# Kernel optimization log

Hardware: AMD Instinct MI355X
Metric: run time of the kernel (lower is better)

The kernel has to match this reference:

```python
import jax, jax.numpy as jnp
import numpy as np

B, T, N = 128, 512, 256


def setup_inputs() -> dict:
    key = jax.random.key(0)
    k1, k2, k3 = jax.random.split(key, 3)
    emissions = jax.random.normal(k1, (B, T, N), dtype=jnp.float32)
    tags = jax.random.randint(k2, (B, T), 0, N, dtype=jnp.int64)
    mask = jnp.ones((B, T), dtype=jnp.float32)
    trans = jax.random.normal(k3, (N, N), dtype=jnp.float32) * 0.1
    return {"emissions": emissions, "tags": tags, "mask": mask, "trans": trans}


def _forward_alg(emissions, trans):
    # score: [B, N] running log-partition per tag
    score0 = emissions[:, 0]

    def step(score, emit_t):  # emit_t: [B, N]
        # nxt: [B, N_prev, N_next]
        nxt = score[:, :, None] + trans[None, :, :] + emit_t[:, None, :]
        return jax.nn.logsumexp(nxt, axis=1), None

    # scan over time (emissions[:, 1:] -> time-major [T-1, B, N])
    score, _ = jax.lax.scan(step, score0, jnp.swapaxes(emissions[:, 1:], 0, 1))
    return jax.nn.logsumexp(score, axis=1)  # [B]


def _score_gold(emissions, tags, mask, trans):
    b = jnp.arange(emissions.shape[0])
    s0 = emissions[b, 0, tags[:, 0]]  # [B]
    # emit scores at gold tags for t >= 1: [B, T-1]
    emit = jnp.take_along_axis(emissions[:, 1:], tags[:, 1:, None], axis=2)[..., 0]
    # transition scores tags[t-1] -> tags[t]: [B, T-1]
    trans_sel = trans[tags[:, :-1], tags[:, 1:]]
    return s0 + jnp.sum((emit + trans_sel) * mask[:, 1:], axis=1)


def reference(emissions, tags, mask, trans):
    # neg_log_likelihood: mean(logZ - gold_score)
    # (the torch.where(mask, score, score) in forward_alg is a no-op and omitted)
    z = _forward_alg(emissions, trans)
    g = _score_gold(emissions, tags, mask, trans)
    return jnp.mean(z - g)
```

## Files before the change

### kernel.cpp

```cpp
#include <hip/hip_runtime.h>

typedef float f4v __attribute__((ext_vector_type(4)));
typedef int   i8v __attribute__((ext_vector_type(8)));

#define LOG2E 1.4426950408889634f
#define LN2   0.6931471805599453f
#define SC1   0x7F7F7F7F

#define SYNC_LDS() __asm__ __volatile__("s_waitcnt lgkmcnt(0)\n\ts_barrier" ::: "memory")

__device__ __forceinline__ float fast_exp2(float x) {
#if __has_builtin(__builtin_amdgcn_exp2f)
    return __builtin_amdgcn_exp2f(x);
#else
    return exp2f(x);
#endif
}

__device__ __forceinline__ unsigned char f2bf8(float x) {
    return (unsigned char)(__builtin_amdgcn_cvt_pk_bf8_f32(x, x, 0, false) & 0xff);
}

__launch_bounds__(256, 1)
__global__ void crf_main(const float* __restrict__ emissions,
                         const float* __restrict__ trans,
                         float* __restrict__ V,  float* __restrict__ W,
                         float* __restrict__ CF, float* __restrict__ CB) {
    const int T = 512, N = 256;
    const bool fwd = blockIdx.x < 128;
    const int b  = fwd ? blockIdx.x : blockIdx.x - 128;
    const int j  = threadIdx.x;
    const int l  = j & 63;
    const int w  = j >> 6;
    const int lg = l >> 4;
    const int ll = l & 15;

    __shared__ alignas(16) unsigned char u_lds[2][256];
    __shared__ float cm2_lds[256];

    if (fwd) {
        const float* tcol = trans + j;
        float m = -1e30f;
        #pragma unroll 8
        for (int i = 0; i < N; ++i) m = fmaxf(m, tcol[i * N]);
        cm2_lds[j] = m * LOG2E;
    } else {
        const float4* trow = (const float4*)(trans + (size_t)j * N);
        float m = -1e30f;
        #pragma unroll 8
        for (int i = 0; i < 64; ++i) {
            float4 t4 = trow[i];
            m = fmaxf(m, fmaxf(fmaxf(t4.x, t4.y), fmaxf(t4.z, t4.w)));
        }
        cm2_lds[j] = m * LOG2E;
    }
    __syncthreads();
    const float cm2 = cm2_lds[j];

    i8v Efr[4][2];
    #pragma unroll
    for (int c = 0; c < 4; ++c) {
        const int   col = 64 * w + 16 * c + ll;
        const float cc  = cm2_lds[col];
        #pragma unroll
        for (int q = 0; q < 2; ++q) {
            i8v ev;
            #pragma unroll
            for (int d = 0; d < 8; ++d) {
                const int k0 = 128 * q + 32 * lg + 4 * d;
                float f0, f1, f2, f3;
                if (fwd) {
                    f0 = fast_exp2(trans[(size_t)(k0 + 0) * N + col] * LOG2E - cc);
                    f1 = fast_exp2(trans[(size_t)(k0 + 1) * N + col] * LOG2E - cc);
                    f2 = fast_exp2(trans[(size_t)(k0 + 2) * N + col] * LOG2E - cc);
                    f3 = fast_exp2(trans[(size_t)(k0 + 3) * N + col] * LOG2E - cc);
                } else {
                    float4 t4 = *(const float4*)(trans + (size_t)col * N + k0);
                    f0 = fast_exp2(t4.x * LOG2E - cc);
                    f1 = fast_exp2(t4.y * LOG2E - cc);
                    f2 = fast_exp2(t4.z * LOG2E - cc);
                    f3 = fast_exp2(t4.w * LOG2E - cc);
                }
                int pk = __builtin_amdgcn_cvt_pk_fp8_f32(f0, f1, 0, false);
                pk     = __builtin_amdgcn_cvt_pk_fp8_f32(f2, f3, pk, true);
                ev[d] = pk;
            }
            Efr[c][q] = ev;
        }
    }

    const float* em_j = emissions + ((size_t)b * T) * N + j;
    u_lds[0][j] = f2bf8(fast_exp2(em_j[(size_t)(fwd ? 0 : 511) * N] * LOG2E));
    float C = 0.f;
    const int NS = fwd ? 255 : 256;
    float em1 = em_j[(size_t)(fwd ? 1 : 510) * N];
    float em2 = em_j[(size_t)(fwd ? 2 : 509) * N];
    SYNC_LDS();

    float vfin = 0.f;

    for (int s = 1; s <= NS; ++s) {
        const int pb = (s - 1) & 1;
        const uint4* ub4 = (const uint4*)u_lds[pb];
        uint4 a0 = ub4[2 * lg],     a1 = ub4[2 * lg + 1];
        uint4 b0 = ub4[8 + 2 * lg], b1 = ub4[8 + 2 * lg + 1];
        i8v ua0, ua1;
        ua0[0]=a0.x; ua0[1]=a0.y; ua0[2]=a0.z; ua0[3]=a0.w;
        ua0[4]=a1.x; ua0[5]=a1.y; ua0[6]=a1.z; ua0[7]=a1.w;
        ua1[0]=b0.x; ua1[1]=b0.y; ua1[2]=b0.z; ua1[3]=b0.w;
        ua1[4]=b1.x; ua1[5]=b1.y; ua1[6]=b1.z; ua1[7]=b1.w;
        const unsigned int u0b = u_lds[pb][0];

        float em = em1;
        em1 = em2;
        em2 = (s + 2 < 256) ? em_j[(size_t)(fwd ? (s + 2) : (509 - s)) * N] : 0.0f;

        const int   eb   = (int)((u0b >> 2) & 0x1fu);
        const int   k    = (eb ? eb : 1) - 15;
        const float r    = __int_as_float((121 - k) << 23);
        const float gain = fast_exp2(fmaf(em, LOG2E, cm2));
        const float sc   = gain * r;

        f4v z = {0.f, 0.f, 0.f, 0.f};
        f4v d0 = z, d1 = z, d2 = z, d3 = z;
        d0 = __builtin_amdgcn_mfma_scale_f32_16x16x128_f8f6f4(ua0, Efr[0][0], d0, 1, 0, 0, SC1, 0, SC1);
        d1 = __builtin_amdgcn_mfma_scale_f32_16x16x128_f8f6f4(ua0, Efr[1][0], d1, 1, 0, 0, SC1, 0, SC1);
        d2 = __builtin_amdgcn_mfma_scale_f32_16x16x128_f8f6f4(ua0, Efr[2][0], d2, 1, 0, 0, SC1, 0, SC1);
        d3 = __builtin_amdgcn_mfma_scale_f32_16x16x128_f8f6f4(ua0, Efr[3][0], d3, 1, 0, 0, SC1, 0, SC1);
        d0 = __builtin_amdgcn_mfma_scale_f32_16x16x128_f8f6f4(ua1, Efr[0][1], d0, 1, 0, 0, SC1, 0, SC1);
        d1 = __builtin_amdgcn_mfma_scale_f32_16x16x128_f8f6f4(ua1, Efr[1][1], d1, 1, 0, 0, SC1, 0, SC1);
        d2 = __builtin_amdgcn_mfma_scale_f32_16x16x128_f8f6f4(ua1, Efr[2][1], d2, 1, 0, 0, SC1, 0, SC1);
        d3 = __builtin_amdgcn_mfma_scale_f32_16x16x128_f8f6f4(ua1, Efr[3][1], d3, 1, 0, 0, SC1, 0, SC1);

        const float A0 = (lg == 0) ? d0[0] : (lg == 1) ? d1[0] : (lg == 2) ? d2[0] : d3[0];

        if (s < NS) {
            C += (float)(k + 6);
            u_lds[s & 1][j] = f2bf8(A0 * sc);
        } else {
            vfin = A0 * gain;
        }
        SYNC_LDS();
    }

    if (fwd) { V[(size_t)b * 256 + j] = vfin; if (j == 0) CF[b] = C; }
    else     { W[(size_t)b * 256 + j] = vfin; if (j == 0) CB[b] = C; }
}

__global__ void crf_combine(const float* __restrict__ emissions,
                            const int*   __restrict__ tags,
                            const float* __restrict__ mask,
                            const float* __restrict__ trans,
                            const float* __restrict__ V,  const float* __restrict__ W,
                            const float* __restrict__ CF, const float* __restrict__ CB,
                            float* __restrict__ ws2) {
    const int T = 512, N = 256;
    const int b = blockIdx.x, j = threadIdx.x;
    __shared__ float red[256];

    red[j] = V[(size_t)b * 256 + j] * W[(size_t)b * 256 + j];
    __syncthreads();
    #pragma unroll
    for (int s = 128; s > 0; s >>= 1) {
        if (j < s) red[j] += red[j + s];
        __syncthreads();
    }
    const float Z = (CF[b] + CB[b] + log2f(red[0])) * LN2;
    __syncthreads();

    float gp = 0.f;
    const int*   tg  = tags + (size_t)b * T;
    const float* mk  = mask + (size_t)b * T;
    const float* emb = emissions + ((size_t)b * T) * N;
    for (int t = 1 + j; t < T; t += 256) {
        int tt = tg[t], tp = tg[t - 1];
        gp += (emb[(size_t)t * N + tt] + trans[(size_t)tp * N + tt]) * mk[t];
    }
    if (j == 0) gp += emb[tg[0]];
    red[j] = gp;
    __syncthreads();
    #pragma unroll
    for (int s = 128; s > 0; s >>= 1) {
        if (j < s) red[j] += red[j + s];
        __syncthreads();
    }
    if (j == 0) ws2[b] = Z - red[0];
}

__global__ void crf_finalize(const float* __restrict__ ws2, float* __restrict__ out) {
    int l = threadIdx.x;
    float s = ws2[l] + ws2[l + 64];
    #pragma unroll
    for (int d = 32; d > 0; d >>= 1) s += __shfl_down(s, d);
    if (l == 0) out[0] = s * (1.0f / 128.0f);
}

extern "C" void kernel_launch(void* const* d_in, const int* in_sizes, int n_in,
                              void* d_out, int out_size, void* d_ws, size_t ws_size,
                              hipStream_t stream) {
    const float* emissions = (const float*)d_in[0];
    const int*   tags      = (const int*)  d_in[1];
    const float* mask      = (const float*)d_in[2];
    const float* trans     = (const float*)d_in[3];
    float* out = (float*)d_out;

    float* wsf = (float*)d_ws;
    float* V   = wsf;
    float* W   = wsf + 32768;
    float* CF  = wsf + 65536;
    float* CB  = wsf + 65664;
    float* ws2 = wsf + 65792;

    crf_main    <<<dim3(256), dim3(256), 0, stream>>>(emissions, trans, V, W, CF, CB);
    crf_combine <<<dim3(128), dim3(256), 0, stream>>>(emissions, tags, mask, trans, V, W, CF, CB, ws2);
    crf_finalize<<<dim3(1),   dim3(64),  0, stream>>>(ws2, out);
}
```

Measured before the change: 132.6 us.

## Fuse finalize into combine kernel via atomic ticket and peel last recurrence step

Merges the combine and finalize kernels into a single tail kernel. The last block to arrive, detected with an atomic counter reset by the main kernel, performs the final mean reduction, which removes one kernel launch. The recurrence loop now peels its final step, so the per-step branch is gone, swaps read/write LDS pointers instead of indexing by parity, unrolls by two, and clamps the emission prefetch index. This adds an atomic and threadfences, and correctness depends on the counter reset in crf_main being ordered before crf_tail runs.

```diff
diff --git a/kernel.cpp b/kernel.cpp
--- a/kernel.cpp
+++ b/kernel.cpp
@@ -25,7 +25,8 @@
 __global__ void crf_main(const float* __restrict__ emissions,
                          const float* __restrict__ trans,
                          float* __restrict__ V,  float* __restrict__ W,
-                         float* __restrict__ CF, float* __restrict__ CB) {
+                         float* __restrict__ CF, float* __restrict__ CB,
+                         int* __restrict__ counter) {
     const int T = 512, N = 256;
     const bool fwd = blockIdx.x < 128;
     const int b  = fwd ? blockIdx.x : blockIdx.x - 128;
@@ -34,6 +35,8 @@
     const int w  = j >> 6;
     const int lg = l >> 4;
     const int ll = l & 15;
+
+    if (blockIdx.x == 0 && j == 0) *counter = 0;
 
     __shared__ alignas(16) unsigned char u_lds[2][256];
     __shared__ float cm2_lds[256];
@@ -97,23 +100,45 @@
     float em2 = em_j[(size_t)(fwd ? 2 : 509) * N];
     SYNC_LDS();
 
-    float vfin = 0.f;
-
-    for (int s = 1; s <= NS; ++s) {
-        const int pb = (s - 1) & 1;
-        const uint4* ub4 = (const uint4*)u_lds[pb];
-        uint4 a0 = ub4[2 * lg],     a1 = ub4[2 * lg + 1];
-        uint4 b0 = ub4[8 + 2 * lg], b1 = ub4[8 + 2 * lg + 1];
-        i8v ua0, ua1;
-        ua0[0]=a0.x; ua0[1]=a0.y; ua0[2]=a0.z; ua0[3]=a0.w;
-        ua0[4]=a1.x; ua0[5]=a1.y; ua0[6]=a1.z; ua0[7]=a1.w;
-        ua1[0]=b0.x; ua1[1]=b0.y; ua1[2]=b0.z; ua1[3]=b0.w;
-        ua1[4]=b1.x; ua1[5]=b1.y; ua1[6]=b1.z; ua1[7]=b1.w;
-        const unsigned int u0b = u_lds[pb][0];
+    const unsigned char* rb = u_lds[0];
+    unsigned char*       wb = u_lds[1];
+
+#define LOAD_UA()                                                              \
+    const uint4* ub4 = (const uint4*)rb;                                       \
+    uint4 a0 = ub4[2 * lg],     a1 = ub4[2 * lg + 1];                          \
+    uint4 b0 = ub4[8 + 2 * lg], b1 = ub4[8 + 2 * lg + 1];                      \
+    i8v ua0, ua1;                                                              \
+    ua0[0]=a0.x; ua0[1]=a0.y; ua0[2]=a0.z; ua0[3]=a0.w;                        \
+    ua0[4]=a1.x; ua0[5]=a1.y; ua0[6]=a1.z; ua0[7]=a1.w;                        \
+    ua1[0]=b0.x; ua1[1]=b0.y; ua1[2]=b0.z; ua1[3]=b0.w;                        \
+    ua1[4]=b1.x; ua1[5]=b1.y; ua1[6]=b1.z; ua1[7]=b1.w;                        \
+    const unsigned int u0b = rb[0];
+
+#define MFMA_BLOCK()                                                                                   \
+    f4v z = {0.f, 0.f, 0.f, 0.f};                                                                      \
+    f4v d0 = z, d1 = z, d2 = z, d3 = z;                                                                \
+    d0 = __builtin_amdgcn_mfma_scale_f32_16x16x128_f8f6f4(ua0, Efr[0][0], d0, 1, 0, 0, SC1, 0, SC1);   \
+    d1 = __builtin_amdgcn_mfma_scale_f32_16x16x128_f8f6f4(ua0, Efr[1][0], d1, 1, 0, 0, SC1, 0, SC1);   \
+    d2 = __builtin_amdgcn_mfma_scale_f32_16x16x128_f8f6f4(ua0, Efr[2][0], d2, 1, 0, 0, SC1, 0, SC1);   \
+    d3 = __builtin_amdgcn_mfma_scale_f32_16x16x128_f8f6f4(ua0, Efr[3][0], d3, 1, 0, 0, SC1, 0, SC1);   \
+    d0 = __builtin_amdgcn_mfma_scale_f32_16x16x128_f8f6f4(ua1, Efr[0][1], d0, 1, 0, 0, SC1, 0, SC1);   \
+    d1 = __builtin_amdgcn_mfma_scale_f32_16x16x128_f8f6f4(ua1, Efr[1][1], d1, 1, 0, 0, SC1, 0, SC1);   \
+    d2 = __builtin_amdgcn_mfma_scale_f32_16x16x128_f8f6f4(ua1, Efr[2][1], d2, 1, 0, 0, SC1, 0, SC1);   \
+    d3 = __builtin_amdgcn_mfma_scale_f32_16x16x128_f8f6f4(ua1, Efr[3][1], d3, 1, 0, 0, SC1, 0, SC1);   \
+    const float A0 = (lg == 0) ? d0[0] : (lg == 1) ? d1[0] : (lg == 2) ? d2[0] : d3[0];
+
+    #pragma unroll 2
+    for (int s = 1; s < NS; ++s) {
+        LOAD_UA();
 
         float em = em1;
         em1 = em2;
-        em2 = (s + 2 < 256) ? em_j[(size_t)(fwd ? (s + 2) : (509 - s)) * N] : 0.0f;
+        {
+            const int  idxf = (s + 2 > 255) ? 255 : (s + 2);
+            const int  idx  = fwd ? idxf : (509 - s);
+            const float emL = em_j[(size_t)idx * N];
+            em2 = (s + 2 < 256) ? emL : 0.0f;
+        }
 
         const int   eb   = (int)((u0b >> 2) & 0x1fu);
         const int   k    = (eb ? eb : 1) - 15;
@@ -121,42 +146,41 @@
         const float gain = fast_exp2(fmaf(em, LOG2E, cm2));
         const float sc   = gain * r;
 
-        f4v z = {0.f, 0.f, 0.f, 0.f};
-        f4v d0 = z, d1 = z, d2 = z, d3 = z;
-        d0 = __builtin_amdgcn_mfma_scale_f32_16x16x128_f8f6f4(ua0, Efr[0][0], d0, 1, 0, 0, SC1, 0, SC1);
-        d1 = __builtin_amdgcn_mfma_scale_f32_16x16x128_f8f6f4(ua0, Efr[1][0], d1, 1, 0, 0, SC1, 0, SC1);
-        d2 = __builtin_amdgcn_mfma_scale_f32_16x16x128_f8f6f4(ua0, Efr[2][0], d2, 1, 0, 0, SC1, 0, SC1);
-        d3 = __builtin_amdgcn_mfma_scale_f32_16x16x128_f8f6f4(ua0, Efr[3][0], d3, 1, 0, 0, SC1, 0, SC1);
-        d0 = __builtin_amdgcn_mfma_scale_f32_16x16x128_f8f6f4(ua1, Efr[0][1], d0, 1, 0, 0, SC1, 0, SC1);
-        d1 = __builtin_amdgcn_mfma_scale_f32_16x16x128_f8f6f4(ua1, Efr[1][1], d1, 1, 0, 0, SC1, 0, SC1);
-        d2 = __builtin_amdgcn_mfma_scale_f32_16x16x128_f8f6f4(ua1, Efr[2][1], d2, 1, 0, 0, SC1, 0, SC1);
-        d3 = __builtin_amdgcn_mfma_scale_f32_16x16x128_f8f6f4(ua1, Efr[3][1], d3, 1, 0, 0, SC1, 0, SC1);
-
-        const float A0 = (lg == 0) ? d0[0] : (lg == 1) ? d1[0] : (lg == 2) ? d2[0] : d3[0];
-
-        if (s < NS) {
-            C += (float)(k + 6);
-            u_lds[s & 1][j] = f2bf8(A0 * sc);
-        } else {
-            vfin = A0 * gain;
-        }
+        MFMA_BLOCK();
+
+        C += (float)(k + 6);
+        wb[j] = f2bf8(A0 * sc);
+        { unsigned char* t = wb; wb = (unsigned char*)rb; rb = t; }
         SYNC_LDS();
+    }
+
+    float vfin;
+    {
+        LOAD_UA();
+        (void)u0b;
+        const float gain = fast_exp2(fmaf(em1, LOG2E, cm2));
+        MFMA_BLOCK();
+        vfin = A0 * gain;
     }
 
     if (fwd) { V[(size_t)b * 256 + j] = vfin; if (j == 0) CF[b] = C; }
     else     { W[(size_t)b * 256 + j] = vfin; if (j == 0) CB[b] = C; }
-}
-
-__global__ void crf_combine(const float* __restrict__ emissions,
-                            const int*   __restrict__ tags,
-                            const float* __restrict__ mask,
-                            const float* __restrict__ trans,
-                            const float* __restrict__ V,  const float* __restrict__ W,
-                            const float* __restrict__ CF, const float* __restrict__ CB,
-                            float* __restrict__ ws2) {
+#undef LOAD_UA
+#undef MFMA_BLOCK
+}
+
+__global__ void crf_tail(const float* __restrict__ emissions,
+                         const int*   __restrict__ tags,
+                         const float* __restrict__ mask,
+                         const float* __restrict__ trans,
+                         const float* __restrict__ V,  const float* __restrict__ W,
+                         const float* __restrict__ CF, const float* __restrict__ CB,
+                         float* __restrict__ ws2, int* __restrict__ counter,
+                         float* __restrict__ out) {
     const int T = 512, N = 256;
     const int b = blockIdx.x, j = threadIdx.x;
     __shared__ float red[256];
+    __shared__ int ticket;
 
     red[j] = V[(size_t)b * 256 + j] * W[(size_t)b * 256 + j];
     __syncthreads();
@@ -184,15 +208,20 @@
         if (j < s) red[j] += red[j + s];
         __syncthreads();
     }
-    if (j == 0) ws2[b] = Z - red[0];
-}
-
-__global__ void crf_finalize(const float* __restrict__ ws2, float* __restrict__ out) {
-    int l = threadIdx.x;
-    float s = ws2[l] + ws2[l + 64];
-    #pragma unroll
-    for (int d = 32; d > 0; d >>= 1) s += __shfl_down(s, d);
-    if (l == 0) out[0] = s * (1.0f / 128.0f);
+    if (j == 0) {
+        ws2[b] = Z - red[0];
+        __threadfence();
+        ticket = atomicAdd(counter, 1);
+    }
+    __syncthreads();
+    if (ticket == 127 && j < 64) {
+        __threadfence();
+        volatile const float* wv = ws2;
+        float s = wv[j] + wv[j + 64];
+        #pragma unroll
+        for (int d = 32; d > 0; d >>= 1) s += __shfl_down(s, d);
+        if (j == 0) out[0] = s * (1.0f / 128.0f);
+    }
 }
 
 extern "C" void kernel_launch(void* const* d_in, const int* in_sizes, int n_in,
@@ -205,13 +234,14 @@
     float* out = (float*)d_out;
 
     float* wsf = (float*)d_ws;
-    float* V   = wsf;
-    float* W   = wsf + 32768;
-    float* CF  = wsf + 65536;
-    float* CB  = wsf + 65664;
-    float* ws2 = wsf + 65792;
-
-    crf_main    <<<dim3(256), dim3(256), 0, stream>>>(emissions, trans, V, W, CF, CB);
-    crf_combine <<<dim3(128), dim3(256), 0, stream>>>(emissions, tags, mask, trans, V, W, CF, CB, ws2);
-    crf_finalize<<<dim3(1),   dim3(64),  0, stream>>>(ws2, out);
-}
+    float* V    = wsf;
+    float* W    = wsf + 32768;
+    float* CF   = wsf + 65536;
+    float* CB   = wsf + 65664;
+    float* ws2  = wsf + 65792;
+    int*   cnt  = (int*)(wsf + 65920);
+
+    crf_main<<<dim3(256), dim3(256), 0, stream>>>(emissions, trans, V, W, CF, CB, cnt);
+    crf_tail<<<dim3(128), dim3(256), 0, stream>>>(emissions, tags, mask, trans,
+                                                  V, W, CF, CB, ws2, cnt, out);
+}
```

Result: slower. 170.2 us (+28.4%).
